# Kernel optimization log

Hardware: AMD Instinct MI355X
Metric: run time of the kernel (lower is better)

## Reference

```python
import jax, jax.numpy as jnp
import numpy as np
import math

B, S, HID, NH, INTER, L = 8, 512, 768, 12, 3072, 4
DH = HID // NH
EPS = 1e-12


def setup_inputs() -> dict:
    key = jax.random.key(0)
    ks = jax.random.split(key, 12)
    s = 0.02
    hidden_states = jax.random.normal(ks[0], (B, S, HID), jnp.float32)
    lengths = jax.random.randint(ks[1], (B,), S // 2, S + 1)
    attention_mask = (jnp.arange(S)[None, :] < lengths[:, None]).astype(jnp.float32)
    return dict(
        hidden_states=hidden_states,
        attention_mask=attention_mask,
        Wqkv_w=jax.random.normal(ks[2], (L, 3 * HID, HID), jnp.float32) * s,
        Wqkv_b=jnp.zeros((L, 3 * HID), jnp.float32),
        attn_out_w=jax.random.normal(ks[3], (L, HID, HID), jnp.float32) * s,
        attn_out_b=jnp.zeros((L, HID), jnp.float32),
        ln1_g=jnp.ones((L, HID), jnp.float32),
        ln1_b=jnp.zeros((L, HID), jnp.float32),
        glu_w=jax.random.normal(ks[4], (L, 2 * INTER, HID), jnp.float32) * s,
        wo_w=jax.random.normal(ks[5], (L, HID, INTER), jnp.float32) * s,
        wo_b=jnp.zeros((L, HID), jnp.float32),
        ln2_g=jnp.ones((L, HID), jnp.float32),
        ln2_b=jnp.zeros((L, HID), jnp.float32),
        r1=1.0 + 0.1 * jax.random.normal(ks[6], (L, NH, 1, 1), jnp.float32),
        r2=1.0 + 0.1 * jax.random.normal(ks[7], (L, NH, 1, 1), jnp.float32),
        r3=1.0 + 0.1 * jax.random.normal(ks[8], (L, NH, 1, 1), jnp.float32),
    )


def _ln(x, g, b):
    mu = x.mean(-1, keepdims=True)
    var = ((x - mu) ** 2).mean(-1, keepdims=True)
    return (x - mu) / jnp.sqrt(var + EPS) * g + b


def _forward(hidden_states, attention_mask, Wqkv_w, Wqkv_b, attn_out_w, attn_out_b,
             ln1_g, ln1_b, glu_w, wo_w, wo_b, ln2_g, ln2_b, r1, r2, r3):
    mask = attention_mask  # [B,S] float, 1=valid
    pos = jnp.arange(S)
    rel = jnp.abs(pos[None, :] - pos[:, None]).astype(jnp.float32)  # [S,S]
    rel_pos = rel > 0
    attn_bias = (1.0 - mask)[:, None, None, :] * -10000.0  # [B,1,1,S]
    # unpad_input <-> zero invalid rows of padded tensor
    h = hidden_states * mask[:, :, None]
    for l in range(L):
        c1 = jnp.clip(r1[l], 1e-7)  # [NH,1,1]
        c2 = jnp.clip(r2[l], 1e-7)
        c3 = jnp.clip(r3[l], 1e-7)
        relp = jnp.where(rel_pos, rel, 1.0) ** c3  # [NH,S,S], safe pow at |i-j|=0
        relp = jnp.where(rel_pos, relp, 0.0)
        kb = -c1 * jnp.log1p(c2 * relp)  # kerple bias [NH,S,S]
        bias = attn_bias + kb[None]  # [B,NH,S,S]
        # qkv on valid tokens only (pad_input reinserts zeros)
        qkv = (h @ Wqkv_w[l].T + Wqkv_b[l]) * mask[:, :, None]
        qkv = qkv.reshape(B, S, 3, NH, DH)
        q = qkv[:, :, 0].transpose(0, 2, 1, 3)  # [B,NH,S,DH]
        k = qkv[:, :, 1].transpose(0, 2, 1, 3)
        v = qkv[:, :, 2].transpose(0, 2, 1, 3)
        scores = jnp.einsum('bhqd,bhkd->bhqk', q, k) / math.sqrt(DH) + bias
        probs = jax.nn.softmax(scores, axis=-1)
        attn = jnp.einsum('bhqk,bhkd->bhqd', probs, v)
        attn = attn.transpose(0, 2, 1, 3).reshape(B, S, HID)
        ao = _ln(attn @ attn_out_w[l].T + attn_out_b[l] + h, ln1_g[l], ln1_b[l])
        ao = ao * mask[:, :, None]
        g = ao @ glu_w[l].T  # [B,S,2*INTER]
        x = jax.nn.gelu(g[..., :INTER], approximate=False) * g[..., INTER:]
        h = _ln(x @ wo_w[l].T + wo_b[l] + ao, ln2_g[l], ln2_b[l])
        h = h * mask[:, :, None]
    return h


def reference(hidden_states, attention_mask, Wqkv_w, Wqkv_b, attn_out_w, attn_out_b,
              ln1_g, ln1_b, glu_w, wo_w, wo_b, ln2_g, ln2_b, r1, r2, r3):
    return _forward(hidden_states, attention_mask, Wqkv_w, Wqkv_b, attn_out_w,
                    attn_out_b, ln1_g, ln1_b, glu_w, wo_w, wo_b, ln2_g, ln2_b,
                    r1, r2, r3)
```

## Files before the change

kernel.cpp:

```cpp
#include <hip/hip_runtime.h>
#include <hip/hip_bf16.h>
#include <math.h>

#define BQ 8
#define SQ 512
#define HID 768
#define NH 12
#define DH 64
#define INTER 3072
#define NL 4
#define M_TOK (BQ*SQ)

typedef unsigned short ushort_t;
typedef __attribute__((ext_vector_type(8))) short bf16x8;
typedef __attribute__((ext_vector_type(8))) unsigned short u16x8;
typedef __attribute__((ext_vector_type(4))) float f32x4;

__device__ __forceinline__ float bf2f(ushort_t u) {
  union { float f; unsigned int i; } v; v.i = ((unsigned int)u) << 16; return v.f;
}
__device__ __forceinline__ ushort_t f2bf(float f) {
  __hip_bfloat16 h = __float2bfloat16(f);
  return *reinterpret_cast<ushort_t*>(&h);
}

__device__ __forceinline__ void gload_lds16(const ushort_t* g, ushort_t* l) {
  __builtin_amdgcn_global_load_lds(
      (const __attribute__((address_space(1))) void*)g,
      (__attribute__((address_space(3))) void*)l, 16, 0, 0);
}

template<int N>
__device__ __forceinline__ void wait_vm() {
  if constexpr (N == 0)      asm volatile("s_waitcnt vmcnt(0)" ::: "memory");
  else if constexpr (N == 6) asm volatile("s_waitcnt vmcnt(6)" ::: "memory");
  else if constexpr (N == 8) asm volatile("s_waitcnt vmcnt(8)" ::: "memory");
  else                       asm volatile("s_waitcnt vmcnt(12)" ::: "memory");
}

__global__ __launch_bounds__(256) void prep_kernel(
    const float* __restrict__ hidden, const float* __restrict__ amask,
    float* __restrict__ maskf, float* __restrict__ maskbias,
    ushort_t* __restrict__ hb)
{
  int i = blockIdx.x * 256 + threadIdx.x;
  if (i < M_TOK * HID) {
    float m = amask[i / HID];
    hb[i] = f2bf(hidden[i] * m);
    if (i < M_TOK) {
      maskf[i] = amask[i];
      maskbias[i] = (1.0f - amask[i]) * (-10000.0f);
    }
  }
}

__global__ void kerple_all_kernel(const float* __restrict__ r1,
                                  const float* __restrict__ r2,
                                  const float* __restrict__ r3,
                                  float* __restrict__ kbt_all)
{
  int lh = blockIdx.x;
  int d  = threadIdx.x;
  float c1 = fmaxf(r1[lh], 1e-7f);
  float c2 = fmaxf(r2[lh], 1e-7f);
  float c3 = fmaxf(r3[lh], 1e-7f);
  float v = 0.0f;
  if (d > 0) v = -c1 * log1pf(c2 * powf((float)d, c3));
  kbt_all[lh * SQ + d] = v;
}

#define WS0 (3*HID*HID)
#define WS1 (HID*HID)
#define WS2 (2*INTER*HID)
#define WS3 (HID*INTER)
#define WTOT (WS0+WS1+WS2+WS3)

__global__ __launch_bounds__(256) void wcast_layer_kernel(
    const float* __restrict__ w0, const float* __restrict__ w1,
    const float* __restrict__ w2, const float* __restrict__ w3,
    ushort_t* __restrict__ dst)
{
  int i = (blockIdx.x * 256 + threadIdx.x) * 4;
  if (i >= WTOT) return;
  const float* src; int off;
  if (i < WS0)                { src = w0; off = i; }
  else if (i < WS0+WS1)       { src = w1; off = i - WS0; }
  else if (i < WS0+WS1+WS2)   { src = w2; off = i - WS0 - WS1; }
  else                        { src = w3; off = i - WS0 - WS1 - WS2; }
  float4 v = *reinterpret_cast<const float4*>(src + off);
  ushort4 o;
  o.x = f2bf(v.x); o.y = f2bf(v.y); o.z = f2bf(v.z); o.w = f2bf(v.w);
  *reinterpret_cast<ushort4*>(dst + i) = o;
}

template<int MF, int NB, int BK, int EPI, int VN, int DB, int WPB>
__global__ __launch_bounds__(256, WPB) void mfma_gemm(
    const ushort_t* __restrict__ A, const ushort_t* __restrict__ B0p,
    const ushort_t* __restrict__ B1p, const float* __restrict__ bias,
    const float* __restrict__ rowscale, ushort_t* __restrict__ Cb,
    int N, int K)
{
  constexpr int BM   = MF * 32;
  constexpr int SMK  = BK / 8 - 1;
  constexpr int SSH  = (BK == 32) ? 1 : 0;
  constexpr int AIS  = (BM * BK * 2) / 4096;
  constexpr int BIS  = (128 * BK * 2) / 4096;
  constexpr int KH   = BK / 32;
  constexpr int NBUF = DB ? 2 : 1;

  __shared__ ushort_t As_[NBUF][BM * BK];
  __shared__ ushort_t Bs_[NBUF][NB][128 * BK];

  int tid = threadIdx.x;
  int lane = tid & 63, w = tid >> 6;
  int wr = w >> 1, wc = w & 1;
  int g = lane >> 4, r = lane & 15;
  int bn = blockIdx.x, bm = blockIdx.y;

  f32x4 acc[NB][MF][4];
#pragma unroll
  for (int p = 0; p < NB; ++p)
#pragma unroll
    for (int m = 0; m < MF; ++m)
#pragma unroll
      for (int n = 0; n < 4; ++n) acc[p][m][n] = (f32x4){0.f, 0.f, 0.f, 0.f};

  const ushort_t* Arow  = A   + (size_t)bm * BM * K;
  const ushort_t* Brow0 = B0p + (size_t)bn * 128 * K;
  const ushort_t* Brow1 = (NB == 2) ? (B1p + (size_t)bn * 128 * K) : nullptr;

  auto stage = [&](const ushort_t* base, ushort_t* lds, int k0, int ISS_w) {
#pragma unroll
    for (int i = 0; i < 4; ++i) {
      if (i >= ISS_w) break;
      int o   = (w * ISS_w + i) * 1024 + lane * 16;
      int row = o / (BK * 2);
      int pc  = (o >> 4) & SMK;
      int lc  = pc ^ ((row >> SSH) & SMK);
      gload_lds16(base + (size_t)row * K + k0 + lc * 8,
                  lds + ((w * ISS_w + i) << 9));
    }
  };
  auto stage_all = [&](int k0, int buf) {
    stage(Arow,  &As_[buf][0],    k0, AIS);
    stage(Brow0, &Bs_[buf][0][0], k0, BIS);
    if constexpr (NB == 2) stage(Brow1, &Bs_[buf][1][0], k0, BIS);
  };
  auto compute = [&](int buf) {
#pragma unroll
    for (int kh = 0; kh < KH; ++kh) {
      bf16x8 af[MF], bf_[4];
#pragma unroll
      for (int m = 0; m < MF; ++m)
        af[m] = *(const bf16x8*)(&As_[buf][(wr * (BM/2) + m * 16 + r) * BK
                  + (((kh * 4 + g) ^ ((r >> SSH) & SMK)) * 8)]);
#pragma unroll
      for (int n = 0; n < 4; ++n)
        bf_[n] = *(const bf16x8*)(&Bs_[buf][0][(wc * 64 + n * 16 + r) * BK
                  + (((kh * 4 + g) ^ ((r >> SSH) & SMK)) * 8)]);
#pragma unroll
      for (int m = 0; m < MF; ++m)
#pragma unroll
        for (int n = 0; n < 4; ++n)
          acc[0][m][n] = __builtin_amdgcn_mfma_f32_16x16x32_bf16(
              af[m], bf_[n], acc[0][m][n], 0, 0, 0);
      if constexpr (NB == 2) {
        bf16x8 bg[4];
#pragma unroll
        for (int n = 0; n < 4; ++n)
          bg[n] = *(const bf16x8*)(&Bs_[buf][1][(wc * 64 + n * 16 + r) * BK
                    + (((kh * 4 + g) ^ ((r >> SSH) & SMK)) * 8)]);
#pragma unroll
        for (int m = 0; m < MF; ++m)
#pragma unroll
          for (int n = 0; n < 4; ++n)
            acc[1][m][n] = __builtin_amdgcn_mfma_f32_16x16x32_bf16(
                af[m], bg[n], acc[1][m][n], 0, 0, 0);
      }
    }
  };

  int NT = K / BK;
  if constexpr (DB) {
    stage_all(0, 0);
    for (int t = 0; t < NT; ++t) {
      int cur = t & 1;
      if (t + 1 < NT) {
        stage_all((t + 1) * BK, cur ^ 1);
        wait_vm<VN>();
      } else {
        wait_vm<0>();
      }
      __builtin_amdgcn_s_barrier();
      compute(cur);
      __builtin_amdgcn_s_barrier();
    }
  } else {
    for (int t = 0; t < NT; ++t) {
      stage_all(t * BK, 0);
      wait_vm<0>();
      __builtin_amdgcn_s_barrier();
      compute(0);
      __builtin_amdgcn_s_barrier();
    }
  }

  int r0 = bm * BM + wr * (BM/2), c0 = bn * 128 + wc * 64;
#pragma unroll
  for (int m = 0; m < MF; ++m)
#pragma unroll
    for (int n = 0; n < 4; ++n) {
      int col  = c0 + n * 16 + (lane & 15);
      int rowb = r0 + m * 16 + (lane >> 4) * 4;
      if constexpr (EPI == 0) {
        float bv = bias ? bias[col] : 0.0f;
#pragma unroll
        for (int j = 0; j < 4; ++j)
          Cb[(size_t)(rowb + j) * N + col] = f2bf(acc[0][m][n][j] + bv);
      } else if constexpr (EPI == 1) {
#pragma unroll
        for (int j = 0; j < 4; ++j) {
          float va = acc[0][m][n][j];
          float vb = acc[1][m][n][j];
          float ge = 0.5f * va * (1.0f + erff(va * 0.70710678118654752440f));
          Cb[(size_t)(rowb + j) * N + col] = f2bf(ge * vb);
        }
      } else {
        float bv = bias ? bias[col] : 0.0f;
#pragma unroll
        for (int j = 0; j < 4; ++j) {
          float v = (acc[0][m][n][j] + bv) * rowscale[rowb + j];
          Cb[(size_t)(rowb + j) * N + col] = f2bf(v);
        }
      }
    }
}

__global__ __launch_bounds__(256) void attn_mfma(
    const ushort_t* __restrict__ qkvb, const float* __restrict__ kbt,
    const float* __restrict__ maskbias, ushort_t* __restrict__ attnb)
{
  __shared__ ushort_t Ks[64 * 64];
  __shared__ ushort_t Vt[64 * 64];
  __shared__ ushort_t Ps[64 * 64];
  __shared__ float    kbs[SQ];
  __shared__ float    mbs[SQ];

  int tid  = threadIdx.x;
  int lane = tid & 63, w = tid >> 6;
  int g = lane >> 4, r = lane & 15;
  int bid = blockIdx.x;
  int qt = (bid >> 3) & 7;
  int t_ = (bid & 7) * 12 + (bid >> 6);
  int hh = t_ % NH;
  int b  = t_ / NH;
  int q0 = qt * 64;

  for (int i = tid; i < SQ; i += 256) {
    kbs[i] = kbt[hh * SQ + i];
    mbs[i] = maskbias[b * SQ + i];
  }

  bf16x8 qf[2];
  {
    const ushort_t* qsrc = qkvb + (size_t)(b * SQ + q0 + w * 16 + r) * (3 * HID)
                         + hh * DH + g * 8;
    qf[0] = *(const bf16x8*)(qsrc);
    qf[1] = *(const bf16x8*)(qsrc + 32);
  }

  float m_run[4], l_run[4];
  f32x4 oacc[4];
#pragma unroll
  for (int j = 0; j < 4; ++j) { m_run[j] = -1e30f; l_run[j] = 0.f; }
#pragma unroll
  for (int nd = 0; nd < 4; ++nd) oacc[nd] = (f32x4){0.f, 0.f, 0.f, 0.f};

  int k2 = (tid & 31) * 2, dg = tid >> 5;

  for (int kc = 0; kc < 8; ++kc) {
    __syncthreads();
#pragma unroll
    for (int ii = 0; ii < 2; ++ii) {
      int row = (w * 2 + ii) * 8 + (lane >> 3);
      int c   = lane & 7;
      const ushort_t* src = qkvb + (size_t)(b * SQ + kc * 64 + row) * (3 * HID)
                          + HID + hh * DH + ((c ^ (row & 7)) * 8);
      gload_lds16(src, Ks + (w * 2 + ii) * 512 + lane * 8);
    }
    {
      const ushort_t* v0 = qkvb + (size_t)(b * SQ + kc * 64 + k2) * (3 * HID)
                         + 2 * HID + hh * DH + dg * 8;
      const ushort_t* v1 = v0 + 3 * HID;
      u16x8 a = *(const u16x8*)v0;
      u16x8 c = *(const u16x8*)v1;
#pragma unroll
      for (int u = 0; u < 8; ++u) {
        int d = dg * 8 + u;
        int addr = d * 64 + (((k2 >> 3) ^ (d & 7)) * 8) + (k2 & 7);
        ushort2 pr; pr.x = (ushort_t)a[u]; pr.y = (ushort_t)c[u];
        *(ushort2*)(Vt + addr) = pr;
      }
    }
    __syncthreads();

    f32x4 sacc[4];
#pragma unroll
    for (int n = 0; n < 4; ++n) sacc[n] = (f32x4){0.f, 0.f, 0.f, 0.f};
    __builtin_amdgcn_s_setprio(1);
#pragma unroll
    for (int kh = 0; kh < 2; ++kh) {
#pragma unroll
      for (int n = 0; n < 4; ++n) {
        bf16x8 kf = *(const bf16x8*)(Ks + (n * 16 + r) * 64
                                     + (((g + kh * 4) ^ (r & 7)) * 8));
        sacc[n] = __builtin_amdgcn_mfma_f32_16x16x32_bf16(qf[kh], kf, sacc[n], 0, 0, 0);
      }
    }
    __builtin_amdgcn_s_setprio(0);

    float sval[4][4], mx[4];
#pragma unroll
    for (int j = 0; j < 4; ++j) mx[j] = -1e30f;
#pragma unroll
    for (int n = 0; n < 4; ++n) {
      int kg = kc * 64 + n * 16 + r;
      float mb = mbs[kg];
#pragma unroll
      for (int j = 0; j < 4; ++j) {
        int qg = q0 + w * 16 + g * 4 + j;
        float s = sacc[n][j] * 0.125f + mb + kbs[abs(qg - kg)];
        sval[n][j] = s;
        mx[j] = fmaxf(mx[j], s);
      }
    }
#pragma unroll
    for (int j = 0; j < 4; ++j) {
      mx[j] = fmaxf(mx[j], __shfl_xor(mx[j], 1));
      mx[j] = fmaxf(mx[j], __shfl_xor(mx[j], 2));
      mx[j] = fmaxf(mx[j], __shfl_xor(mx[j], 4));
      mx[j] = fmaxf(mx[j], __shfl_xor(mx[j], 8));
      float mn = fmaxf(m_run[j], mx[j]);
      mx[j] = __expf(m_run[j] - mn);
      m_run[j] = mn;
    }
    float rs[4] = {0.f, 0.f, 0.f, 0.f};
#pragma unroll
    for (int n = 0; n < 4; ++n) {
#pragma unroll
      for (int j = 0; j < 4; ++j) {
        float pp = __expf(sval[n][j] - m_run[j]);
        int prow = w * 16 + g * 4 + j;
        int pcol = n * 16 + r;
        Ps[prow * 64 + (((pcol >> 3) ^ (prow & 7)) * 8) + (pcol & 7)] = f2bf(pp);
        rs[j] += pp;
      }
    }
#pragma unroll
    for (int j = 0; j < 4; ++j) {
      rs[j] += __shfl_xor(rs[j], 1);
      rs[j] += __shfl_xor(rs[j], 2);
      rs[j] += __shfl_xor(rs[j], 4);
      rs[j] += __shfl_xor(rs[j], 8);
      l_run[j] = l_run[j] * mx[j] + rs[j];
    }
#pragma unroll
    for (int nd = 0; nd < 4; ++nd)
#pragma unroll
      for (int j = 0; j < 4; ++j) oacc[nd][j] *= mx[j];

    __builtin_amdgcn_s_setprio(1);
#pragma unroll
    for (int kh = 0; kh < 2; ++kh) {
      bf16x8 pa = *(const bf16x8*)(Ps + (w * 16 + r) * 64
                                   + (((g + kh * 4) ^ (r & 7)) * 8));
#pragma unroll
      for (int nd = 0; nd < 4; ++nd) {
        bf16x8 vf = *(const bf16x8*)(Vt + (nd * 16 + r) * 64
                                     + (((g + kh * 4) ^ (r & 7)) * 8));
        oacc[nd] = __builtin_amdgcn_mfma_f32_16x16x32_bf16(pa, vf, oacc[nd], 0, 0, 0);
      }
    }
    __builtin_amdgcn_s_setprio(0);
  }

#pragma unroll
  for (int j = 0; j < 4; ++j) {
    float inv = 1.0f / l_run[j];
    int token = b * SQ + q0 + w * 16 + g * 4 + j;
#pragma unroll
    for (int nd = 0; nd < 4; ++nd)
      attnb[(size_t)token * HID + hh * DH + nd * 16 + r] = f2bf(oacc[nd][j] * inv);
  }
}

__global__ __launch_bounds__(256) void ln_res_kernel(
    const ushort_t* __restrict__ t, const ushort_t* __restrict__ res,
    const float* __restrict__ g, const float* __restrict__ bb,
    const float* __restrict__ maskf, float* __restrict__ outf,
    ushort_t* __restrict__ outb)
{
  __shared__ float part[8];
  int row = blockIdx.x, tid = threadIdx.x;
  int wid = tid >> 6;
  const ushort_t* tp = t   + (size_t)row * HID;
  const ushort_t* rp = res + (size_t)row * HID;
  float y0 = bf2f(tp[tid      ]) + bf2f(rp[tid      ]);
  float y1 = bf2f(tp[tid + 256]) + bf2f(rp[tid + 256]);
  float y2 = bf2f(tp[tid + 512]) + bf2f(rp[tid + 512]);

  float s = y0 + y1 + y2;
  s += __shfl_xor(s, 1);  s += __shfl_xor(s, 2);  s += __shfl_xor(s, 4);
  s += __shfl_xor(s, 8);  s += __shfl_xor(s, 16); s += __shfl_xor(s, 32);
  if ((tid & 63) == 0) part[wid] = s;
  __syncthreads();
  float mu = (part[0] + part[1] + part[2] + part[3]) * (1.0f / 768.0f);

  float d0 = y0 - mu, d1 = y1 - mu, d2 = y2 - mu;
  float v = d0*d0 + d1*d1 + d2*d2;
  v += __shfl_xor(v, 1);  v += __shfl_xor(v, 2);  v += __shfl_xor(v, 4);
  v += __shfl_xor(v, 8);  v += __shfl_xor(v, 16); v += __shfl_xor(v, 32);
  if ((tid & 63) == 0) part[4 + wid] = v;
  __syncthreads();
  float rstd = rsqrtf((part[4] + part[5] + part[6] + part[7]) * (1.0f / 768.0f)
                      + 1e-12f);
  float mk = maskf[row];
  float v0 = (d0*rstd*g[tid      ] + bb[tid      ]) * mk;
  float v1 = (d1*rstd*g[tid + 256] + bb[tid + 256]) * mk;
  float v2 = (d2*rstd*g[tid + 512] + bb[tid + 512]) * mk;
  size_t base = (size_t)row * HID;
  outb[base + tid      ] = f2bf(v0);
  outb[base + tid + 256] = f2bf(v1);
  outb[base + tid + 512] = f2bf(v2);
  if (outf) {
    outf[base + tid      ] = v0;
    outf[base + tid + 256] = v1;
    outf[base + tid + 512] = v2;
  }
}

extern "C" void kernel_launch(void* const* d_in, const int* in_sizes, int n_in,
                              void* d_out, int out_size, void* d_ws, size_t ws_size,
                              hipStream_t stream) {
  const float* hidden     = (const float*)d_in[0];
  const float* amask      = (const float*)d_in[1];
  const float* Wqkv_w     = (const float*)d_in[2];
  const float* Wqkv_b     = (const float*)d_in[3];
  const float* attn_out_w = (const float*)d_in[4];
  const float* attn_out_b = (const float*)d_in[5];
  const float* ln1_g      = (const float*)d_in[6];
  const float* ln1_b      = (const float*)d_in[7];
  const float* glu_w      = (const float*)d_in[8];
  const float* wo_w       = (const float*)d_in[9];
  const float* wo_b       = (const float*)d_in[10];
  const float* ln2_g      = (const float*)d_in[11];
  const float* ln2_b      = (const float*)d_in[12];
  const float* r1         = (const float*)d_in[13];
  const float* r2         = (const float*)d_in[14];
  const float* r3         = (const float*)d_in[15];

  float* ws       = (float*)d_ws;
  float* maskf    = ws;
  float* maskbias = maskf    + 4096;
  float* kbt_all  = maskbias + 4096;
  ushort_t* us    = (ushort_t*)(kbt_all + NL*NH*SQ);
  ushort_t* hb    = us;
  ushort_t* aob   = hb    + (size_t)M_TOK*HID;
  ushort_t* atnb  = aob   + (size_t)M_TOK*HID;
  ushort_t* tb    = atnb  + (size_t)M_TOK*HID;
  ushort_t* qkv_b = tb    + (size_t)M_TOK*HID;
  ushort_t* xb    = qkv_b + (size_t)M_TOK*3*HID;
  ushort_t* wbf   = xb    + (size_t)M_TOK*INTER;

  prep_kernel<<<(M_TOK*HID + 255)/256, 256, 0, stream>>>(
      hidden, amask, maskf, maskbias, hb);
  kerple_all_kernel<<<NL*NH, SQ, 0, stream>>>(r1, r2, r3, kbt_all);

  for (int l = 0; l < NL; ++l) {
    wcast_layer_kernel<<<(WTOT/4 + 255)/256, 256, 0, stream>>>(
        Wqkv_w     + (size_t)l*WS0,
        attn_out_w + (size_t)l*WS1,
        glu_w      + (size_t)l*WS2,
        wo_w       + (size_t)l*WS3, wbf);
    ushort_t* wqkv = wbf;
    ushort_t* wao  = wbf + WS0;
    ushort_t* wga  = wbf + WS0 + WS1;
    ushort_t* wgb  = wga + (size_t)INTER*HID;
    ushort_t* wwo  = wbf + WS0 + WS1 + WS2;

    mfma_gemm<4,1,64,2,8,1,2><<<dim3(3*HID/128, M_TOK/128), 256, 0, stream>>>(
        hb, wqkv, nullptr, Wqkv_b + (size_t)l*3*HID, maskf, qkv_b, 3*HID, HID);

    attn_mfma<<<BQ*NH*8, 256, 0, stream>>>(
        qkv_b, kbt_all + (size_t)l*NH*SQ, maskbias, atnb);

    mfma_gemm<2,1,64,0,6,1,2><<<dim3(HID/128, M_TOK/64), 256, 0, stream>>>(
        atnb, wao, nullptr, attn_out_b + (size_t)l*HID, nullptr, tb, HID, HID);

    ln_res_kernel<<<M_TOK, 256, 0, stream>>>(tb, hb, ln1_g + (size_t)l*HID,
                                             ln1_b + (size_t)l*HID, maskf,
                                             nullptr, aob);

    mfma_gemm<2,2,64,1,0,0,4><<<dim3(INTER/128, M_TOK/64), 256, 0, stream>>>(
        aob, wga, wgb, nullptr, nullptr, xb, INTER, HID);

    mfma_gemm<2,1,64,0,6,1,2><<<dim3(HID/128, M_TOK/64), 256, 0, stream>>>(
        xb, wwo, nullptr, wo_b + (size_t)l*HID, nullptr, tb, HID, INTER);

    float* hout = (l == NL - 1) ? (float*)d_out : nullptr;
    ln_res_kernel<<<M_TOK, 256, 0, stream>>>(tb, aob, ln2_g + (size_t)l*HID,
                                             ln2_b + (size_t)l*HID, maskf,
                                             hout, hb);
  }
}
```

Before: 766.2 us.

## Double-buffer K/V tiles in attention and retile QKV GEMM to 64-row blocks

The attention kernel now uses two LDS buffers for K and V. It issues the next chunk's K global-to-LDS load and V register load before computing on the current chunk, then writes V into the other buffer after the PV MFMAs. This is meant to hide global memory latency behind the QK^T/softmax/PV work, at the cost of doubled LDS for K/V, which may lower occupancy. Separately, the QKV projection GEMM switches to a 64-row tile configuration with twice as many blocks.

```diff
diff --git a/kernel.cpp b/kernel.cpp
--- a/kernel.cpp
+++ b/kernel.cpp
@@ -240,8 +240,8 @@
     const ushort_t* __restrict__ qkvb, const float* __restrict__ kbt,
     const float* __restrict__ maskbias, ushort_t* __restrict__ attnb)
 {
-  __shared__ ushort_t Ks[64 * 64];
-  __shared__ ushort_t Vt[64 * 64];
+  __shared__ ushort_t Ks[2][64 * 64];
+  __shared__ ushort_t Vt[2][64 * 64];
   __shared__ ushort_t Ps[64 * 64];
   __shared__ float    kbs[SQ];
   __shared__ float    mbs[SQ];
@@ -278,31 +278,45 @@
 
   int k2 = (tid & 31) * 2, dg = tid >> 5;
 
-  for (int kc = 0; kc < 8; ++kc) {
-    __syncthreads();
+  auto issue_K = [&](int kc, int buf) {
 #pragma unroll
     for (int ii = 0; ii < 2; ++ii) {
       int row = (w * 2 + ii) * 8 + (lane >> 3);
       int c   = lane & 7;
       const ushort_t* src = qkvb + (size_t)(b * SQ + kc * 64 + row) * (3 * HID)
                           + HID + hh * DH + ((c ^ (row & 7)) * 8);
-      gload_lds16(src, Ks + (w * 2 + ii) * 512 + lane * 8);
-    }
-    {
-      const ushort_t* v0 = qkvb + (size_t)(b * SQ + kc * 64 + k2) * (3 * HID)
-                         + 2 * HID + hh * DH + dg * 8;
-      const ushort_t* v1 = v0 + 3 * HID;
-      u16x8 a = *(const u16x8*)v0;
-      u16x8 c = *(const u16x8*)v1;
-#pragma unroll
-      for (int u = 0; u < 8; ++u) {
-        int d = dg * 8 + u;
-        int addr = d * 64 + (((k2 >> 3) ^ (d & 7)) * 8) + (k2 & 7);
-        ushort2 pr; pr.x = (ushort_t)a[u]; pr.y = (ushort_t)c[u];
-        *(ushort2*)(Vt + addr) = pr;
-      }
-    }
-    __syncthreads();
+      gload_lds16(src, &Ks[buf][(w * 2 + ii) * 512 + lane * 8]);
+    }
+  };
+  u16x8 va, vc;
+  auto load_V = [&](int kc) {
+    const ushort_t* v0 = qkvb + (size_t)(b * SQ + kc * 64 + k2) * (3 * HID)
+                       + 2 * HID + hh * DH + dg * 8;
+    va = *(const u16x8*)v0;
+    vc = *(const u16x8*)(v0 + 3 * HID);
+  };
+  auto write_V = [&](int buf) {
+#pragma unroll
+    for (int u = 0; u < 8; ++u) {
+      int d = dg * 8 + u;
+      int addr = d * 64 + (((k2 >> 3) ^ (d & 7)) * 8) + (k2 & 7);
+      ushort2 pr; pr.x = (ushort_t)va[u]; pr.y = (ushort_t)vc[u];
+      *(ushort2*)(&Vt[buf][addr]) = pr;
+    }
+  };
+
+  issue_K(0, 0);
+  load_V(0);
+  wait_vm<0>();
+  write_V(0);
+  __syncthreads();
+
+  for (int kc = 0; kc < 8; ++kc) {
+    int cur = kc & 1, nxt = cur ^ 1;
+    if (kc + 1 < 8) {
+      issue_K(kc + 1, nxt);
+      load_V(kc + 1);
+    }
 
     f32x4 sacc[4];
 #pragma unroll
@@ -312,8 +326,8 @@
     for (int kh = 0; kh < 2; ++kh) {
 #pragma unroll
       for (int n = 0; n < 4; ++n) {
-        bf16x8 kf = *(const bf16x8*)(Ks + (n * 16 + r) * 64
-                                     + (((g + kh * 4) ^ (r & 7)) * 8));
+        bf16x8 kf = *(const bf16x8*)(&Ks[cur][(n * 16 + r) * 64
+                                     + (((g + kh * 4) ^ (r & 7)) * 8)]);
         sacc[n] = __builtin_amdgcn_mfma_f32_16x16x32_bf16(qf[kh], kf, sacc[n], 0, 0, 0);
       }
     }
@@ -376,12 +390,16 @@
                                    + (((g + kh * 4) ^ (r & 7)) * 8));
 #pragma unroll
       for (int nd = 0; nd < 4; ++nd) {
-        bf16x8 vf = *(const bf16x8*)(Vt + (nd * 16 + r) * 64
-                                     + (((g + kh * 4) ^ (r & 7)) * 8));
+        bf16x8 vf = *(const bf16x8*)(&Vt[cur][(nd * 16 + r) * 64
+                                     + (((g + kh * 4) ^ (r & 7)) * 8)]);
         oacc[nd] = __builtin_amdgcn_mfma_f32_16x16x32_bf16(pa, vf, oacc[nd], 0, 0, 0);
       }
     }
     __builtin_amdgcn_s_setprio(0);
+
+    wait_vm<0>();
+    if (kc + 1 < 8) write_V(nxt);
+    __syncthreads();
   }
 
 #pragma unroll
@@ -488,7 +506,7 @@
     ushort_t* wgb  = wga + (size_t)INTER*HID;
     ushort_t* wwo  = wbf + WS0 + WS1 + WS2;
 
-    mfma_gemm<4,1,64,2,8,1,2><<<dim3(3*HID/128, M_TOK/128), 256, 0, stream>>>(
+    mfma_gemm<2,1,64,2,6,1,2><<<dim3(3*HID/128, M_TOK/64), 256, 0, stream>>>(
         hb, wqkv, nullptr, Wqkv_b + (size_t)l*3*HID, maskf, qkv_b, 3*HID, HID);
 
     attn_mfma<<<BQ*NH*8, 256, 0, stream>>>(
```

Result: faster. 738.1 us (-3.7%).
